# Optimization experiments

Hardware: AMD Instinct MI355X
Metric: run time of the kernel (lower is better)

## Reference

```python
import jax, jax.numpy as jnp
import numpy as np

B = 131072
IN_C = 10
N = 512
HEAD_DIMS = [N, 128, 64, 32, 16, 1]
N_HEADS = 8


def _init_linear(key, fan_in, fan_out, batch=None):
    kw, kb = jax.random.split(key)
    shape_w = (fan_in, fan_out) if batch is None else (batch, fan_in, fan_out)
    shape_b = (fan_out,) if batch is None else (batch, fan_out)
    lim = 1.0 / np.sqrt(fan_in)
    W = jax.random.uniform(kw, shape_w, jnp.float32, -lim, lim)
    b = jax.random.uniform(kb, shape_b, jnp.float32, -lim, lim)
    return W, b


def setup_inputs() -> dict:
    key = jax.random.key(0)
    keys = jax.random.split(key, 10)
    x = jax.random.normal(keys[0], (B, IN_C), jnp.float32)
    W1, b1 = _init_linear(keys[1], 3 * IN_C, N)
    W2, b2 = _init_linear(keys[2], N, N)
    W3, b3 = _init_linear(keys[3], N, N - 3 * IN_C)
    W4, b4 = _init_linear(keys[4], N, N)
    inp = {"x": x, "W1": W1, "b1": b1, "W2": W2, "b2": b2,
           "W3": W3, "b3": b3, "W4": W4, "b4": b4}
    # 8 identical-shaped heads stacked into grouped weights [8, in, out]
    for i in range(5):
        HW, Hb = _init_linear(keys[5 + i], HEAD_DIMS[i], HEAD_DIMS[i + 1], batch=N_HEADS)
        inp[f"HW{i+1}"] = HW
        inp[f"Hb{i+1}"] = Hb
    return inp


def reference(x, W1, b1, W2, b2, W3, b3, W4, b4,
              HW1, Hb1, HW2, Hb2, HW3, Hb3, HW4, Hb4, HW5, Hb5):
    # backbone
    x_skip = jnp.concatenate([x, jnp.sin(x), jnp.cos(x)], axis=-1)  # [B, 3c]
    h = jax.nn.relu(x_skip @ W1 + b1)
    h = jax.nn.relu(h @ W2 + b2)
    h = h @ W3 + b3                                                  # [B, N-3c]
    h = jax.nn.relu(jnp.concatenate([h, x_skip], axis=1))            # [B, N]
    h = h @ W4 + b4  # NOTE: original discards the relu here (no assignment)
    # 8 heads as grouped batched GEMMs: y[g] = head_g(h)
    y = jax.nn.relu(jnp.einsum('bd,gde->gbe', h, HW1) + Hb1[:, None, :])
    y = jax.nn.relu(jnp.einsum('gbd,gde->gbe', y, HW2) + Hb2[:, None, :])
    y = jax.nn.relu(jnp.einsum('gbd,gde->gbe', y, HW3) + Hb3[:, None, :])
    y = jax.nn.relu(jnp.einsum('gbd,gde->gbe', y, HW4) + Hb4[:, None, :])
    y = jnp.einsum('gbd,gde->gbe', y, HW5) + Hb5[:, None, :]         # [8, B, 1]
    return jnp.transpose(y[..., 0])                                  # [B, 8]
```

## Files before the change

kernel.cpp:

```cpp
#include <hip/hip_runtime.h>
#include <hip/hip_bf16.h>

typedef short s16x8 __attribute__((ext_vector_type(8)));
typedef float f32x4 __attribute__((ext_vector_type(4)));
typedef unsigned short u16;
typedef unsigned int u32;

#define TB 64
#define NTHREADS 512

#define P_L1 0
#define P_L2 16384
#define P_L3 278528
#define P_L4 540672
#define P_H1 802816
#define P_H2 1327104
#define P_H3 1392640
#define P_H4 1409024
#define P_TOT 1413120

#define H_OFF   0
#define XS_OFF  65536
#define Y1_OFF  73728
#define LDS_BYTES 139264

__device__ __forceinline__ u16 f2bf(float v) {
  __hip_bfloat16 b = __float2bfloat16(v);
  return __builtin_bit_cast(u16, b);
}
__device__ __forceinline__ float bf2f(u16 u) {
  u32 x = ((u32)u) << 16;
  return __builtin_bit_cast(float, x);
}

template<int FN>
__device__ __forceinline__ void loadB(s16x8 (&b)[FN], const char* unit,
                                      int nCols, int bColBase, int kg, int l15) {
#pragma unroll
  for (int fj = 0; fj < FN; ++fj) {
    const int n = bColBase + fj * 16 + l15;
    b[fj] = *reinterpret_cast<const s16x8*>(unit + (kg * nCols + n) * 16);
  }
}

template<int FM, int FN>
__device__ __forceinline__ void mfma_step(
    const char* lds, int aOff, int aRB, int kByte, int mBase, int l15,
    const s16x8 (&b)[FN], f32x4 (&acc)[FM][FN]) {
  s16x8 a[FM];
#pragma unroll
  for (int fi = 0; fi < FM; ++fi) {
    const int m = mBase + fi * 16 + l15;
    a[fi] = *reinterpret_cast<const s16x8*>(
        lds + aOff + m * aRB + (kByte ^ (((m & 7) << 4) & (aRB - 1))));
  }
#pragma unroll
  for (int fi = 0; fi < FM; ++fi)
#pragma unroll
    for (int fj = 0; fj < FN; ++fj)
      acc[fi][fj] = __builtin_amdgcn_mfma_f32_16x16x32_bf16(a[fi], b[fj], acc[fi][fj], 0, 0, 0);
}

template<int FM, int FN, int KSTEPS>
__device__ __forceinline__ void gemm_reg(
    const char* lds, int aOff, int aRB, int aColBase, int mBase,
    const char* bGlob, int unitStride, int nCols, int bColBase,
    int kg, int l15, f32x4 (&acc)[FM][FN]) {
#pragma unroll
  for (int i = 0; i < FM; ++i)
#pragma unroll
    for (int j = 0; j < FN; ++j) { f32x4 z = {0.f,0.f,0.f,0.f}; acc[i][j] = z; }
  s16x8 bA[FN], bB[FN];
  loadB<FN>(bA, bGlob, nCols, bColBase, kg, l15);
#pragma unroll
  for (int ks = 0; ks < KSTEPS; ks += 2) {
    if (ks + 1 < KSTEPS)
      loadB<FN>(bB, bGlob + (size_t)(ks + 1) * unitStride, nCols, bColBase, kg, l15);
    mfma_step<FM, FN>(lds, aOff, aRB, (aColBase + ks * 32 + kg * 8) * 2,
                      mBase, l15, bA, acc);
    if (ks + 1 < KSTEPS) {
      if (ks + 2 < KSTEPS)
        loadB<FN>(bA, bGlob + (size_t)(ks + 2) * unitStride, nCols, bColBase, kg, l15);
      mfma_step<FM, FN>(lds, aOff, aRB, (aColBase + (ks + 1) * 32 + kg * 8) * 2,
                        mBase, l15, bB, acc);
    }
  }
}

__device__ __forceinline__ void epi_bb(char* lds, const f32x4 (&acc)[4][4],
    const float* bias, int biasLim, bool relu, bool concatXS, int tid)
{
  const int lane = tid & 63;
  const int l15 = lane & 15, rgrp = lane >> 4;
  const int wid = tid >> 6;
#pragma unroll
  for (int fj = 0; fj < 4; ++fj) {
    const int gc = wid * 64 + fj * 16 + l15;
    const float bv = (gc < biasLim) ? bias[gc] : 0.f;
#pragma unroll
    for (int fi = 0; fi < 4; ++fi) {
#pragma unroll
      for (int r = 0; r < 4; ++r) {
        const int m = fi * 16 + rgrp * 4 + r;
        float v = acc[fi][fj][r] + bv;
        if (relu) v = fmaxf(v, 0.f);
        u16 hv = f2bf(v);
        if (concatXS && gc >= 482) {
          const int c2 = gc - 482;
          const float xv = bf2f(*reinterpret_cast<const u16*>(
              lds + XS_OFF + m * 128 + ((c2 * 2) ^ ((m & 7) << 4))));
          hv = f2bf(fmaxf(xv, 0.f));
        }
        *reinterpret_cast<u16*>(lds + H_OFF + m * 1024 + ((gc * 2) ^ ((m & 7) << 4))) = hv;
      }
    }
  }
}

__global__ __launch_bounds__(256)
void prep_weights(const float* __restrict__ W1, const float* __restrict__ W2,
                  const float* __restrict__ W3, const float* __restrict__ W4,
                  const float* __restrict__ HW1, const float* __restrict__ HW2,
                  const float* __restrict__ HW3, const float* __restrict__ HW4,
                  u16* __restrict__ wp)
{
  for (int idx = blockIdx.x * blockDim.x + threadIdx.x; idx < P_TOT;
       idx += gridDim.x * blockDim.x) {
    float v;
    if (idx < P_L2) {
      const int e = idx;
      const int kg = e >> 12, n = (e >> 3) & 511, j = e & 7;
      const int k = kg * 8 + j;
      v = (k < 30) ? W1[k * 512 + n] : 0.f;
    } else if (idx < P_L3) {
      const int e = idx - P_L2;
      const int u = e >> 14, r = e & 16383;
      const int kg = r >> 12, n = (r >> 3) & 511, j = r & 7;
      const int k = u * 32 + kg * 8 + j;
      v = W2[k * 512 + n];
    } else if (idx < P_L4) {
      const int e = idx - P_L3;
      const int u = e >> 14, r = e & 16383;
      const int kg = r >> 12, n = (r >> 3) & 511, j = r & 7;
      const int k = u * 32 + kg * 8 + j;
      v = (n < 482) ? W3[k * 482 + n] : 0.f;
    } else if (idx < P_H1) {
      const int e = idx - P_L4;
      const int u = e >> 14, r = e & 16383;
      const int kg = r >> 12, n = (r >> 3) & 511, j = r & 7;
      const int k = u * 32 + kg * 8 + j;
      v = W4[k * 512 + n];
    } else if (idx < P_H2) {
      const int e = idx - P_H1;
      const int p = e >> 17, r = e & 131071;
      const int u = r >> 13, q = r & 8191;
      const int kg = q >> 11, n = (q >> 3) & 255, j = q & 7;
      const int k = u * 32 + kg * 8 + j;
      const int g = 2 * p + (n >> 7), col = n & 127;
      v = HW1[((size_t)g * 512 + k) * 128 + col];
    } else if (idx < P_H3) {
      const int e = idx - P_H2;
      const int p = e >> 14, r = e & 16383;
      const int u = r >> 12, q = r & 4095;
      const int kg = q >> 10, n = (q >> 3) & 127, j = q & 7;
      const int k = u * 32 + kg * 8 + j;
      const int g = 2 * p + (n >> 6), col = n & 63;
      v = HW2[((size_t)g * 128 + k) * 64 + col];
    } else if (idx < P_H4) {
      const int e = idx - P_H3;
      const int p = e >> 12, r = e & 4095;
      const int u = r >> 11, q = r & 2047;
      const int kg = q >> 9, n = (q >> 3) & 63, j = q & 7;
      const int k = u * 32 + kg * 8 + j;
      const int g = 2 * p + (n >> 5), col = n & 31;
      v = HW3[((size_t)g * 64 + k) * 32 + col];
    } else {
      const int e = idx - P_H4;
      const int p = e >> 10, q = e & 1023;
      const int kg = q >> 8, n = (q >> 3) & 31, j = q & 7;
      const int k = kg * 8 + j;
      const int g = 2 * p + (n >> 4), col = n & 15;
      v = HW4[((size_t)g * 32 + k) * 16 + col];
    }
    wp[idx] = f2bf(v);
  }
}

__global__ __launch_bounds__(NTHREADS, 2)
void fused_mlp(const float* __restrict__ x, const u16* __restrict__ wp,
               const float* __restrict__ b1, const float* __restrict__ b2,
               const float* __restrict__ b3, const float* __restrict__ b4,
               const float* __restrict__ Hb1, const float* __restrict__ Hb2,
               const float* __restrict__ Hb3, const float* __restrict__ Hb4,
               const float* __restrict__ hw5, const float* __restrict__ Hb5,
               float* __restrict__ out)
{
  extern __shared__ char lds[];
  const int tid = threadIdx.x;
  const int lane = tid & 63;
  const int l15 = lane & 15;
  const int rgrp = lane >> 4;
  const int kg = lane >> 4;
  const int wid = tid >> 6;
  const int row0 = blockIdx.x * TB;
  const char* wpB = reinterpret_cast<const char*>(wp);

  for (int i = tid; i < TB * 10; i += NTHREADS) {
    const int r = i / 10, c = i % 10;
    const float xv = x[(size_t)(row0 + r) * 10 + c];
    const int sw = (r & 7) << 4;
    char* rowp = lds + XS_OFF + r * 128;
    *reinterpret_cast<u16*>(rowp + ((c * 2) ^ sw)) = f2bf(xv);
    *reinterpret_cast<u16*>(rowp + (((c + 10) * 2) ^ sw)) = f2bf(__sinf(xv));
    *reinterpret_cast<u16*>(rowp + (((c + 20) * 2) ^ sw)) = f2bf(__cosf(xv));
  }
  for (int i = tid; i < TB * 2; i += NTHREADS) {
    const int r = i >> 1, c = 30 + (i & 1);
    *reinterpret_cast<u16*>(lds + XS_OFF + r * 128 + ((c * 2) ^ ((r & 7) << 4))) = 0;
  }
  __syncthreads();

  {
    f32x4 acc[4][4];
    gemm_reg<4, 4, 1>(lds, XS_OFF, 128, 0, 0,
                      wpB + (size_t)P_L1 * 2, 8192, 512, wid * 64, kg, l15, acc);
    epi_bb(lds, acc, b1, 512, true, false, tid);
    __syncthreads();
  }
  {
    f32x4 acc[4][4];
    gemm_reg<4, 4, 16>(lds, H_OFF, 1024, 0, 0,
                       wpB + (size_t)P_L2 * 2, 32768, 512, wid * 64, kg, l15, acc);
    __syncthreads();
    epi_bb(lds, acc, b2, 512, true, false, tid);
    __syncthreads();
  }
  {
    f32x4 acc[4][4];
    gemm_reg<4, 4, 16>(lds, H_OFF, 1024, 0, 0,
                       wpB + (size_t)P_L3 * 2, 32768, 512, wid * 64, kg, l15, acc);
    __syncthreads();
    epi_bb(lds, acc, b3, 482, true, true, tid);
    __syncthreads();
  }
  {
    f32x4 acc[4][4];
    gemm_reg<4, 4, 16>(lds, H_OFF, 1024, 0, 0,
                       wpB + (size_t)P_L4 * 2, 32768, 512, wid * 64, kg, l15, acc);
    __syncthreads();
    epi_bb(lds, acc, b4, 512, false, false, tid);
    __syncthreads();
  }

  {
    const int half = wid & 1;
    const int mB = half * 32;
    for (int grp = 0; grp < 2; ++grp) {
      if (grp) __syncthreads();

      {
        const int h4 = wid >> 1, colhalf = wid & 1;
        const int g1 = grp * 4 + h4;
        const int pair1 = g1 >> 1, side1 = g1 & 1;
        const int y1o1 = Y1_OFF + (g1 & 3) * 16384;
        f32x4 acc[4][4];
        gemm_reg<4, 4, 16>(lds, H_OFF, 1024, 0, 0,
                           wpB + (size_t)P_H1 * 2 + (size_t)pair1 * 262144, 16384, 256,
                           side1 * 128 + colhalf * 64, kg, l15, acc);
#pragma unroll
        for (int fj = 0; fj < 4; ++fj) {
          const int c = colhalf * 64 + fj * 16 + l15;
          const float bv = Hb1[g1 * 128 + c];
#pragma unroll
          for (int fi = 0; fi < 4; ++fi)
#pragma unroll
            for (int r = 0; r < 4; ++r) {
              const int m = fi * 16 + rgrp * 4 + r;
              const float v = fmaxf(acc[fi][fj][r] + bv, 0.f);
              *reinterpret_cast<u16*>(lds + y1o1 + m * 256 + ((c * 2) ^ ((m & 7) << 4))) = f2bf(v);
            }
        }
      }
      __syncthreads();

      const int g = grp * 4 + (wid >> 1);
      const int pair = g >> 1, side = g & 1;
      const int y1o = Y1_OFF + (g & 3) * 16384;
      const int scrOff = y1o + half * 8192;
      char* scr = lds + scrOff;

      {
        f32x4 a2[2][4];
        gemm_reg<2, 4, 4>(lds, scrOff, 256, 0, 0,
                          wpB + (size_t)P_H2 * 2 + (size_t)pair * 32768, 8192, 128,
                          side * 64, kg, l15, a2);
#pragma unroll
        for (int fj = 0; fj < 4; ++fj) {
          const int c = fj * 16 + l15;
          const float bv = Hb2[g * 64 + c];
#pragma unroll
          for (int fi = 0; fi < 2; ++fi)
#pragma unroll
            for (int r = 0; r < 4; ++r) {
              const int rl = fi * 16 + rgrp * 4 + r;
              const float v = fmaxf(a2[fi][fj][r] + bv, 0.f);
              *reinterpret_cast<u16*>(scr + rl * 256 + ((c * 2) ^ ((rl & 7) << 4))) = f2bf(v);
            }
        }
      }
      {
        f32x4 a3[2][2];
        gemm_reg<2, 2, 2>(lds, scrOff, 256, 0, 0,
                          wpB + (size_t)P_H3 * 2 + (size_t)pair * 8192, 4096, 64,
                          side * 32, kg, l15, a3);
#pragma unroll
        for (int fj = 0; fj < 2; ++fj) {
          const int c = fj * 16 + l15;
          const float bv = Hb3[g * 32 + c];
#pragma unroll
          for (int fi = 0; fi < 2; ++fi)
#pragma unroll
            for (int r = 0; r < 4; ++r) {
              const int rl = fi * 16 + rgrp * 4 + r;
              const float v = fmaxf(a3[fi][fj][r] + bv, 0.f);
              *reinterpret_cast<u16*>(scr + rl * 256 + ((c * 2) ^ ((rl & 7) << 4))) = f2bf(v);
            }
        }
      }
      {
        f32x4 a4[2][1];
        gemm_reg<2, 1, 1>(lds, scrOff, 256, 0, 0,
                          wpB + (size_t)P_H4 * 2 + (size_t)pair * 2048, 2048, 32,
                          side * 16, kg, l15, a4);
        const int c = l15;
        const float bv = Hb4[g * 16 + c];
#pragma unroll
        for (int fi = 0; fi < 2; ++fi)
#pragma unroll
          for (int r = 0; r < 4; ++r) {
            const int rl = fi * 16 + rgrp * 4 + r;
            const float v = fmaxf(a4[fi][0][r] + bv, 0.f);
            *reinterpret_cast<u16*>(scr + rl * 256 + ((c * 2) ^ ((rl & 7) << 4))) = f2bf(v);
          }
      }
      {
        const int r = lane & 31, kh = lane >> 5;
        const s16x8 y4v = *reinterpret_cast<const s16x8*>(
            scr + r * 256 + ((kh * 16) ^ ((r & 7) << 4)));
        float partial = 0.f;
#pragma unroll
        for (int j = 0; j < 8; ++j)
          partial += bf2f((u16)y4v[j]) * hw5[g * 16 + kh * 8 + j];
        partial += __shfl_xor(partial, 32, 64);
        if (kh == 0)
          out[(size_t)(row0 + mB + r) * 8 + g] = Hb5[g] + partial;
      }
    }
  }
}

extern "C" void kernel_launch(void* const* d_in, const int* in_sizes, int n_in,
                              void* d_out, int out_size, void* d_ws, size_t ws_size,
                              hipStream_t stream) {
  (void)in_sizes; (void)n_in; (void)out_size; (void)ws_size;
  const float* x   = (const float*)d_in[0];
  const float* W1  = (const float*)d_in[1];
  const float* b1  = (const float*)d_in[2];
  const float* W2  = (const float*)d_in[3];
  const float* b2  = (const float*)d_in[4];
  const float* W3  = (const float*)d_in[5];
  const float* b3  = (const float*)d_in[6];
  const float* W4  = (const float*)d_in[7];
  const float* b4  = (const float*)d_in[8];
  const float* HW1 = (const float*)d_in[9];
  const float* Hb1 = (const float*)d_in[10];
  const float* HW2 = (const float*)d_in[11];
  const float* Hb2 = (const float*)d_in[12];
  const float* HW3 = (const float*)d_in[13];
  const float* Hb3 = (const float*)d_in[14];
  const float* HW4 = (const float*)d_in[15];
  const float* Hb4 = (const float*)d_in[16];
  const float* HW5 = (const float*)d_in[17];
  const float* Hb5 = (const float*)d_in[18];
  float* out = (float*)d_out;
  u16* wp = (u16*)d_ws;

  prep_weights<<<2048, 256, 0, stream>>>(W1, W2, W3, W4, HW1, HW2, HW3, HW4, wp);

  hipFuncSetAttribute((const void*)fused_mlp,
                      hipFuncAttributeMaxDynamicSharedMemorySize, LDS_BYTES);
  fused_mlp<<<131072 / TB, NTHREADS, LDS_BYTES, stream>>>(
      x, wp, b1, b2, b3, b4, Hb1, Hb2, Hb3, Hb4, HW5, Hb5, out);
}
```

Measured before the change: 395.6 us.

## Fold linear layer W4 into head layer 1 weights and bias

Because the fourth backbone layer has no activation, its weight and bias are precomputed into the first head layer, producing a combined 512x1024 weight and fused bias via two small preprocessing kernels. The main kernel skips the L4 GEMM entirely and uses ping-pong LDS buffers, removing one barrier. This reduces per-row matmul work but introduces an extra bf16 rounding on the fused weight, which may change numerics slightly.

After: 443.3 us. +12.0%, slower.

```diff
diff --git a/kernel.cpp b/kernel.cpp
--- a/kernel.cpp
+++ b/kernel.cpp
@@ -18,10 +18,11 @@
 #define P_H3 1392640
 #define P_H4 1409024
 #define P_TOT 1413120
-
-#define H_OFF   0
-#define XS_OFF  65536
-#define Y1_OFF  73728
+#define P_F  1413120
+
+#define BUF0   0
+#define XS_OFF 65536
+#define BUF1   73728
 #define LDS_BYTES 139264
 
 __device__ __forceinline__ u16 f2bf(float v) {
@@ -88,7 +89,7 @@
 }
 
 __device__ __forceinline__ void epi_bb(char* lds, const f32x4 (&acc)[4][4],
-    const float* bias, int biasLim, bool relu, bool concatXS, int tid)
+    int outOff, const float* bias, int biasLim, bool relu, bool concatXS, int tid)
 {
   const int lane = tid & 63;
   const int l15 = lane & 15, rgrp = lane >> 4;
@@ -111,7 +112,7 @@
               lds + XS_OFF + m * 128 + ((c2 * 2) ^ ((m & 7) << 4))));
           hv = f2bf(fmaxf(xv, 0.f));
         }
-        *reinterpret_cast<u16*>(lds + H_OFF + m * 1024 + ((gc * 2) ^ ((m & 7) << 4))) = hv;
+        *reinterpret_cast<u16*>(lds + outOff + m * 1024 + ((gc * 2) ^ ((m & 7) << 4))) = hv;
       }
     }
   }
@@ -186,12 +187,65 @@
   }
 }
 
+__global__ __launch_bounds__(256)
+void fuse_bias(const float* __restrict__ b4, const float* __restrict__ HW1,
+               const float* __restrict__ Hb1, u16* __restrict__ wp)
+{
+  const int gc = blockIdx.x * 256 + threadIdx.x;
+  const int g = gc >> 7, c = gc & 127;
+  float acc = Hb1[g * 128 + c];
+  for (int j = 0; j < 512; ++j)
+    acc += b4[j] * HW1[((size_t)g * 512 + j) * 128 + c];
+  reinterpret_cast<float*>(wp + P_L4)[gc] = acc;
+}
+
+__global__ __launch_bounds__(512, 2)
+void fuse_w4h1(const float* __restrict__ W4, u16* __restrict__ wp)
+{
+  extern __shared__ char lds[];
+  const int tid = threadIdx.x;
+  const int lane = tid & 63;
+  const int l15 = lane & 15, rgrp = lane >> 4, kg = lane >> 4;
+  const int wid = tid >> 6;
+  const int kb = blockIdx.x * 64;
+  const char* wpB = reinterpret_cast<const char*>(wp);
+
+  for (int i = tid; i < 64 * 512; i += 512) {
+    const int r = i >> 9, t = i & 511;
+    *reinterpret_cast<u16*>(lds + r * 1024 + ((t * 2) ^ ((r & 7) << 4))) =
+        f2bf(W4[(size_t)(kb + r) * 512 + t]);
+  }
+  __syncthreads();
+
+  for (int pass = 0; pass < 2; ++pass) {
+    const int gcW = (pass * 8 + wid) * 64;
+    const int p = gcW >> 8, nb = gcW & 255;
+    f32x4 acc[4][4];
+    gemm_reg<4, 4, 16>(lds, 0, 1024, 0, 0,
+                       wpB + (size_t)P_H1 * 2 + (size_t)p * 262144, 16384, 256, nb,
+                       kg, l15, acc);
+#pragma unroll
+    for (int fj = 0; fj < 4; ++fj) {
+      const int gc = gcW + fj * 16 + l15;
+#pragma unroll
+      for (int fi = 0; fi < 4; ++fi)
+#pragma unroll
+        for (int r = 0; r < 4; ++r) {
+          const int jin = kb + fi * 16 + rgrp * 4 + r;
+          const size_t elem = (size_t)P_F + (size_t)(jin >> 5) * 32768 +
+                              (size_t)(((jin >> 3) & 3) * 1024 + gc) * 8 + (jin & 7);
+          wp[elem] = f2bf(acc[fi][fj][r]);
+        }
+    }
+  }
+}
+
 __global__ __launch_bounds__(NTHREADS, 2)
 void fused_mlp(const float* __restrict__ x, const u16* __restrict__ wp,
                const float* __restrict__ b1, const float* __restrict__ b2,
-               const float* __restrict__ b3, const float* __restrict__ b4,
-               const float* __restrict__ Hb1, const float* __restrict__ Hb2,
-               const float* __restrict__ Hb3, const float* __restrict__ Hb4,
+               const float* __restrict__ b3,
+               const float* __restrict__ Hb2, const float* __restrict__ Hb3,
+               const float* __restrict__ Hb4,
                const float* __restrict__ hw5, const float* __restrict__ Hb5,
                float* __restrict__ out)
 {
@@ -204,6 +258,7 @@
   const int wid = tid >> 6;
   const int row0 = blockIdx.x * TB;
   const char* wpB = reinterpret_cast<const char*>(wp);
+  const float* biasF = reinterpret_cast<const float*>(wp + P_L4);
 
   for (int i = tid; i < TB * 10; i += NTHREADS) {
     const int r = i / 10, c = i % 10;
@@ -224,60 +279,50 @@
     f32x4 acc[4][4];
     gemm_reg<4, 4, 1>(lds, XS_OFF, 128, 0, 0,
                       wpB + (size_t)P_L1 * 2, 8192, 512, wid * 64, kg, l15, acc);
-    epi_bb(lds, acc, b1, 512, true, false, tid);
+    epi_bb(lds, acc, BUF0, b1, 512, true, false, tid);
     __syncthreads();
   }
   {
     f32x4 acc[4][4];
-    gemm_reg<4, 4, 16>(lds, H_OFF, 1024, 0, 0,
+    gemm_reg<4, 4, 16>(lds, BUF0, 1024, 0, 0,
                        wpB + (size_t)P_L2 * 2, 32768, 512, wid * 64, kg, l15, acc);
-    __syncthreads();
-    epi_bb(lds, acc, b2, 512, true, false, tid);
+    epi_bb(lds, acc, BUF1, b2, 512, true, false, tid);
     __syncthreads();
   }
   {
     f32x4 acc[4][4];
-    gemm_reg<4, 4, 16>(lds, H_OFF, 1024, 0, 0,
+    gemm_reg<4, 4, 16>(lds, BUF1, 1024, 0, 0,
                        wpB + (size_t)P_L3 * 2, 32768, 512, wid * 64, kg, l15, acc);
     __syncthreads();
-    epi_bb(lds, acc, b3, 482, true, true, tid);
+    epi_bb(lds, acc, BUF0, b3, 482, true, true, tid);
     __syncthreads();
   }
+
   {
-    f32x4 acc[4][4];
-    gemm_reg<4, 4, 16>(lds, H_OFF, 1024, 0, 0,
-                       wpB + (size_t)P_L4 * 2, 32768, 512, wid * 64, kg, l15, acc);
-    __syncthreads();
-    epi_bb(lds, acc, b4, 512, false, false, tid);
-    __syncthreads();
-  }
-
-  {
+    const int h4 = wid >> 1, chalf = wid & 1;
     const int half = wid & 1;
     const int mB = half * 32;
     for (int grp = 0; grp < 2; ++grp) {
       if (grp) __syncthreads();
 
       {
-        const int h4 = wid >> 1, colhalf = wid & 1;
         const int g1 = grp * 4 + h4;
-        const int pair1 = g1 >> 1, side1 = g1 & 1;
-        const int y1o1 = Y1_OFF + (g1 & 3) * 16384;
+        const int gc0 = g1 * 128 + chalf * 64;
         f32x4 acc[4][4];
-        gemm_reg<4, 4, 16>(lds, H_OFF, 1024, 0, 0,
-                           wpB + (size_t)P_H1 * 2 + (size_t)pair1 * 262144, 16384, 256,
-                           side1 * 128 + colhalf * 64, kg, l15, acc);
+        gemm_reg<4, 4, 16>(lds, BUF0, 1024, 0, 0,
+                           wpB + (size_t)P_F * 2, 65536, 1024, gc0, kg, l15, acc);
+        const int y1o = BUF1 + (g1 & 3) * 16384;
 #pragma unroll
         for (int fj = 0; fj < 4; ++fj) {
-          const int c = colhalf * 64 + fj * 16 + l15;
-          const float bv = Hb1[g1 * 128 + c];
+          const int ch = chalf * 64 + fj * 16 + l15;
+          const float bv = biasF[g1 * 128 + ch];
 #pragma unroll
           for (int fi = 0; fi < 4; ++fi)
 #pragma unroll
             for (int r = 0; r < 4; ++r) {
               const int m = fi * 16 + rgrp * 4 + r;
               const float v = fmaxf(acc[fi][fj][r] + bv, 0.f);
-              *reinterpret_cast<u16*>(lds + y1o1 + m * 256 + ((c * 2) ^ ((m & 7) << 4))) = f2bf(v);
+              *reinterpret_cast<u16*>(lds + y1o + m * 256 + ((ch * 2) ^ ((m & 7) << 4))) = f2bf(v);
             }
         }
       }
@@ -285,8 +330,7 @@
 
       const int g = grp * 4 + (wid >> 1);
       const int pair = g >> 1, side = g & 1;
-      const int y1o = Y1_OFF + (g & 3) * 16384;
-      const int scrOff = y1o + half * 8192;
+      const int scrOff = BUF1 + (g & 3) * 16384 + half * 8192;
       char* scr = lds + scrOff;
 
       {
@@ -386,9 +430,13 @@
   u16* wp = (u16*)d_ws;
 
   prep_weights<<<2048, 256, 0, stream>>>(W1, W2, W3, W4, HW1, HW2, HW3, HW4, wp);
+  fuse_bias<<<4, 256, 0, stream>>>(b4, HW1, Hb1, wp);
+  hipFuncSetAttribute((const void*)fuse_w4h1,
+                      hipFuncAttributeMaxDynamicSharedMemorySize, 65536);
+  fuse_w4h1<<<8, 512, 65536, stream>>>(W4, wp);
 
   hipFuncSetAttribute((const void*)fused_mlp,
                       hipFuncAttributeMaxDynamicSharedMemorySize, LDS_BYTES);
   fused_mlp<<<131072 / TB, NTHREADS, LDS_BYTES, stream>>>(
-      x, wp, b1, b2, b3, b4, Hb1, Hb2, Hb3, Hb4, HW5, Hb5, out);
-}
+      x, wp, b1, b2, b3, Hb2, Hb3, Hb4, HW5, Hb5, out);
+}
```
